# Kernel tuning notes

Hardware: AMD Instinct MI355X
Metric: run time of the kernel (lower is better)

Reference implementation:

```python
import jax, jax.numpy as jnp
import numpy as np

N_TOPICS = 256
BATCH = 131072


def setup_inputs() -> dict:
    key = jax.random.key(0)
    k = jax.random.split(key, 6)
    n, b = N_TOPICS, BATCH
    s = 1.0 / np.sqrt(n)  # matches torch RNNCell uniform(-1/sqrt(h), 1/sqrt(h)) scale
    return {
        "z": jax.random.normal(k[0], (b, n), jnp.float32),
        "h0": jax.random.uniform(k[1], (1, n), jnp.float32),
        "W_ih": jax.random.uniform(k[2], (n, n), jnp.float32, -s, s),
        "W_hh": jax.random.uniform(k[3], (n, n), jnp.float32, -s, s),
        "b_ih": jax.random.uniform(k[4], (n,), jnp.float32, -s, s),
        "b_hh": jax.random.uniform(k[5], (n,), jnp.float32, -s, s),
    }


def _stick_breaking(x):
    # torch.distributions.StickBreakingTransform._call
    D = x.shape[-1]
    offset = jnp.arange(D, 0, -1, dtype=x.dtype)          # [D, D-1, ..., 1]
    zc = jax.nn.sigmoid(x - jnp.log(offset))
    fi = jnp.finfo(x.dtype)
    zc = jnp.clip(zc, fi.tiny, 1.0 - fi.eps)              # _clipped_sigmoid
    z_cumprod = jnp.cumprod(1.0 - zc, axis=-1)
    ones = jnp.ones(x.shape[:-1] + (1,), x.dtype)
    return jnp.concatenate([zc, ones], -1) * jnp.concatenate([ones, z_cumprod], -1)


def reference(z, h0, W_ih, W_hh, b_ih, b_hh):
    n = W_ih.shape[0]
    D = n - 1
    b = b_ih + b_hh
    # step 0: rnncell(h0) with zero hidden state -> tanh(h0 @ W_ih.T + b_ih + b_hh)
    h1 = jnp.tanh(h0 @ W_ih.T + b)                        # (1, n)
    # steps i>0: rnncell(h, h) = tanh(h @ (W_ih + W_hh).T + b_ih + b_hh)
    Wc = (W_ih + W_hh).T

    def step(h, _):
        hn = jnp.tanh(h @ Wc + b)
        return hn, hn

    _, hs = jax.lax.scan(step, h1, None, length=D - 1)    # (D-1, 1, n)
    H = jnp.concatenate([h1[None], hs], axis=0)[:, 0, :]  # (D, n)
    eta = jax.nn.sigmoid(H @ z.T).T                       # (batch, D)
    return _stick_breaking(eta)                           # (batch, n)
```

## Files before the change

### kernel.cpp

```cpp
#include <hip/hip_runtime.h>

#define NTOP 256

typedef __attribute__((ext_vector_type(8))) short bf16x8;
typedef __attribute__((ext_vector_type(4))) float f32x4;

__device__ inline unsigned int packbf(float x) {
  unsigned int u = __float_as_uint(x);
  unsigned int r = (u + 0x7fffu + ((u >> 16) & 1u)) & 0xffff0000u;
  float res = x - __uint_as_float(r);
  unsigned int u2 = __float_as_uint(res);
  unsigned int r2 = u2 + 0x7fffu + ((u2 >> 16) & 1u);
  return r | (r2 >> 16);
}

__device__ inline float tanh_fast(float x) {
  float e = __expf(2.f * x);
  return 1.f - 2.f / (e + 1.f);
}

template <int CTRL>
__device__ inline float dpp_f(float v) {
  return __int_as_float(__builtin_amdgcn_update_dpp(
      0, __float_as_int(v), CTRL, 0xf, 0xf, true));
}

__global__ __launch_bounds__(1024)
__attribute__((amdgpu_waves_per_eu(4, 4)))
void rsbc_recur(
    const float* __restrict__ Wih, const float* __restrict__ Whh,
    const float* __restrict__ bih, const float* __restrict__ bhh,
    const float* __restrict__ h0, unsigned int* __restrict__ Hpack) {
  __shared__ float hA[4][68], hB[4][68];
  const int tid = threadIdx.x;
  const int j = tid >> 2, qt = tid & 3, k0 = qt * 64;
  const float bj = bih[j] + bhh[j];

  float4 w[16];
  {
    const float4* wp = reinterpret_cast<const float4*>(Wih + j * NTOP + k0);
#pragma unroll
    for (int q = 0; q < 16; ++q) w[q] = wp[q];
  }
  if (tid < NTOP) hA[tid >> 6][tid & 63] = h0[tid];
  __syncthreads();

  {
    const float* hq = hA[qt];
    float a0 = 0.f, a1 = 0.f, a2 = 0.f, a3 = 0.f;
#pragma unroll
    for (int q = 0; q < 16; ++q) {
      float4 hv = *reinterpret_cast<const float4*>(hq + 4 * q);
      a0 = fmaf(hv.x, w[q].x, a0);
      a1 = fmaf(hv.y, w[q].y, a1);
      a2 = fmaf(hv.z, w[q].z, a2);
      a3 = fmaf(hv.w, w[q].w, a3);
    }
    float sv = (a0 + a1) + (a2 + a3);
    sv += dpp_f<0xB1>(sv);
    sv += dpp_f<0x4E>(sv);
    if (qt == 0) {
      float v = tanh_fast(sv + bj);
      hB[j >> 6][j & 63] = v;
      Hpack[j] = packbf(v);
    }
  }
  {
    const float4* wq = reinterpret_cast<const float4*>(Whh + j * NTOP + k0);
#pragma unroll
    for (int q = 0; q < 16; ++q) {
      float4 t = wq[q];
      w[q].x += t.x; w[q].y += t.y; w[q].z += t.z; w[q].w += t.w;
    }
  }
  __syncthreads();

#pragma unroll 1
  for (int s = 1; s < 255; ++s) {
    const float(*hr)[68] = (s & 1) ? hB : hA;
    float(*hw)[68] = (s & 1) ? hA : hB;
    const float* hq = hr[qt];
    float a0 = 0.f, a1 = 0.f, a2 = 0.f, a3 = 0.f;
#pragma unroll
    for (int q = 0; q < 16; ++q) {
      float4 hv = *reinterpret_cast<const float4*>(hq + 4 * q);
      a0 = fmaf(hv.x, w[q].x, a0);
      a1 = fmaf(hv.y, w[q].y, a1);
      a2 = fmaf(hv.z, w[q].z, a2);
      a3 = fmaf(hv.w, w[q].w, a3);
    }
    float sv = (a0 + a1) + (a2 + a3);
    sv += dpp_f<0xB1>(sv);
    sv += dpp_f<0x4E>(sv);
    if (qt == 0) {
      float v = tanh_fast(sv + bj);
      hw[j >> 6][j & 63] = v;
      Hpack[s * NTOP + j] = packbf(v);
    }
    __syncthreads();
  }
}

__global__ __launch_bounds__(512)
__attribute__((amdgpu_waves_per_eu(2, 2)))
void rsbc_gemm_sb(
    const float* __restrict__ z, const unsigned int* __restrict__ Hpack,
    float* __restrict__ out) {
  constexpr int AS = 72;
  constexpr int BS = 72;
  constexpr int ES = 260;
  __shared__ __align__(16) char smem[135168];
  __shared__ float logtab[256];
  ushort* Ahi = reinterpret_cast<ushort*>(smem);
  ushort* Alo = Ahi + 128 * AS;
  ushort* Bhi = Alo + 128 * AS;
  ushort* Blo = Bhi + 256 * BS;
  float* eta = reinterpret_cast<float*>(smem);
  float* segT = eta + 128 * ES;

  const int tid = threadIdx.x;
  const size_t row0 = (size_t)blockIdx.x * 128;
  const int wid = tid >> 6, lane = tid & 63;
  const int wr = wid >> 2, wc = wid & 3;
  const int l15 = lane & 15, l4 = lane >> 4;

  if (tid < 255) logtab[tid] = logf((float)(255 - tid));

  f32x4 acc[4][4];
#pragma unroll
  for (int mt = 0; mt < 4; ++mt)
#pragma unroll
    for (int nt = 0; nt < 4; ++nt) acc[mt][nt] = (f32x4){0.f, 0.f, 0.f, 0.f};

  for (int kc = 0; kc < 4; ++kc) {
    const int kb = kc * 64;
    float4 zreg[4];
#pragma unroll
    for (int it = 0; it < 4; ++it) {
      int idx = tid + 512 * it;
      int r = idx >> 4, q = idx & 15;
      zreg[it] = *reinterpret_cast<const float4*>(
          z + (row0 + r) * NTOP + kb + 4 * q);
    }
    uint4 hreg[8];
#pragma unroll
    for (int it = 0; it < 8; ++it) {
      int idx = tid + 512 * it;
      int r = idx >> 4, q = idx & 15;
      hreg[it] = (r < 255)
                     ? *reinterpret_cast<const uint4*>(
                           Hpack + r * NTOP + kb + 4 * q)
                     : make_uint4(0u, 0u, 0u, 0u);
    }
    __syncthreads();
#pragma unroll
    for (int it = 0; it < 4; ++it) {
      int idx = tid + 512 * it;
      int r = idx >> 4, q = idx & 15;
      float4 v = zreg[it];
      unsigned int p0 = packbf(v.x), p1 = packbf(v.y),
                   p2 = packbf(v.z), p3 = packbf(v.w);
      *reinterpret_cast<ushort4*>(&Ahi[r * AS + 4 * q]) = make_ushort4(
          (ushort)(p0 >> 16), (ushort)(p1 >> 16),
          (ushort)(p2 >> 16), (ushort)(p3 >> 16));
      *reinterpret_cast<ushort4*>(&Alo[r * AS + 4 * q]) = make_ushort4(
          (ushort)(p0 & 0xffff), (ushort)(p1 & 0xffff),
          (ushort)(p2 & 0xffff), (ushort)(p3 & 0xffff));
    }
#pragma unroll
    for (int it = 0; it < 8; ++it) {
      int idx = tid + 512 * it;
      int r = idx >> 4, q = idx & 15;
      uint4 hv = hreg[it];
      *reinterpret_cast<ushort4*>(&Bhi[r * BS + 4 * q]) = make_ushort4(
          (ushort)(hv.x >> 16), (ushort)(hv.y >> 16),
          (ushort)(hv.z >> 16), (ushort)(hv.w >> 16));
      *reinterpret_cast<ushort4*>(&Blo[r * BS + 4 * q]) = make_ushort4(
          (ushort)(hv.x & 0xffff), (ushort)(hv.y & 0xffff),
          (ushort)(hv.z & 0xffff), (ushort)(hv.w & 0xffff));
    }
    __syncthreads();
#pragma unroll
    for (int ks = 0; ks < 2; ++ks) {
      const int ko = ks * 32 + l4 * 8;
      bf16x8 afh[4], afl[4], bfh[4], bfl[4];
#pragma unroll
      for (int mt = 0; mt < 4; ++mt) {
        int r = 64 * wr + 16 * mt + l15;
        afh[mt] = *reinterpret_cast<const bf16x8*>(&Ahi[r * AS + ko]);
        afl[mt] = *reinterpret_cast<const bf16x8*>(&Alo[r * AS + ko]);
      }
#pragma unroll
      for (int nt = 0; nt < 4; ++nt) {
        int n = 64 * wc + 16 * nt + l15;
        bfh[nt] = *reinterpret_cast<const bf16x8*>(&Bhi[n * BS + ko]);
        bfl[nt] = *reinterpret_cast<const bf16x8*>(&Blo[n * BS + ko]);
      }
#pragma unroll
      for (int mt = 0; mt < 4; ++mt)
#pragma unroll
        for (int nt = 0; nt < 4; ++nt) {
          acc[mt][nt] = __builtin_amdgcn_mfma_f32_16x16x32_bf16(
              afh[mt], bfh[nt], acc[mt][nt], 0, 0, 0);
          acc[mt][nt] = __builtin_amdgcn_mfma_f32_16x16x32_bf16(
              afh[mt], bfl[nt], acc[mt][nt], 0, 0, 0);
          acc[mt][nt] = __builtin_amdgcn_mfma_f32_16x16x32_bf16(
              afl[mt], bfh[nt], acc[mt][nt], 0, 0, 0);
        }
    }
  }
  __syncthreads();

#pragma unroll
  for (int mt = 0; mt < 4; ++mt) {
    int rbase = 64 * wr + 16 * mt + 4 * l4;
#pragma unroll
    for (int nt = 0; nt < 4; ++nt) {
      int c = 64 * wc + 16 * nt + l15;
#pragma unroll
      for (int i = 0; i < 4; ++i) {
        float x = acc[mt][nt][i];
        eta[(rbase + i) * ES + c] = 1.f / (1.f + __expf(-x));
      }
    }
  }
  __syncthreads();

  const int r = tid >> 2, qk = tid & 3;
  const int kbeg = 64 * qk, kend = (qk == 3) ? 255 : 64 * qk + 64;
  float* er = &eta[r * ES];
  {
    float cp = 1.f;
#pragma unroll 4
    for (int k = kbeg; k < kend; ++k) {
      float x = er[k] - logtab[k];
      float zc = 1.f / (1.f + __expf(-x));
      zc = fminf(fmaxf(zc, 1.1754943508222875e-38f), 0.99999988079071045f);
      er[k] = zc * cp;
      cp *= 1.f - zc;
    }
    segT[r * 4 + qk] = cp;
  }
  __syncthreads();
  {
    float p = 1.f;
    if (qk > 0) p *= segT[r * 4 + 0];
    if (qk > 1) p *= segT[r * 4 + 1];
    if (qk > 2) p *= segT[r * 4 + 2];
    if (qk > 0) {
#pragma unroll 4
      for (int k = kbeg; k < kend; ++k) er[k] *= p;
    }
    if (qk == 3) er[255] = p * segT[r * 4 + 3];
  }
  __syncthreads();

#pragma unroll
  for (int it = 0; it < 16; ++it) {
    int idx = tid + 512 * it;
    int rr = idx >> 6, cq = idx & 63;
    float4 vv = *reinterpret_cast<const float4*>(&eta[rr * ES + 4 * cq]);
    *reinterpret_cast<float4*>(&out[(row0 + rr) * NTOP + 4 * cq]) = vv;
  }
}

extern "C" void kernel_launch(void* const* d_in, const int* in_sizes, int n_in,
                              void* d_out, int out_size, void* d_ws, size_t ws_size,
                              hipStream_t stream) {
  const float* z   = (const float*)d_in[0];
  const float* h0  = (const float*)d_in[1];
  const float* Wih = (const float*)d_in[2];
  const float* Whh = (const float*)d_in[3];
  const float* bih = (const float*)d_in[4];
  const float* bhh = (const float*)d_in[5];
  float* out = (float*)d_out;
  unsigned int* Hpack = (unsigned int*)d_ws;

  rsbc_recur<<<1, 1024, 0, stream>>>(Wih, Whh, bih, bhh, h0, Hpack);
  const int nrows = out_size / NTOP;
  const int blocks = nrows / 128;
  rsbc_gemm_sb<<<blocks, 512, 0, stream>>>(z, Hpack, out);
}
```

Baseline: 323.2 us.

## Restructure recurrence thread mapping and shrink GEMM tiles for higher occupancy

The recurrence kernel now has each 16-lane group compute four output neurons over 16-element K slices. It reduces with a 16-lane DPP tree and uses a padded, swizzled shared-memory layout for h. This is meant to cut per-step LDS reads and the serial latency of the 254-step recurrence. The GEMM+stick-breaking kernel moves to 64-row tiles with a 32-wide K step, halving shared memory per block to allow 4 waves per EU. This trades more blocks and more K iterations, each with its own barriers, for higher occupancy and better latency hiding. The stick-breaking scan is split into 8 segments per row instead of 4.

```diff
diff --git a/kernel.cpp b/kernel.cpp
--- a/kernel.cpp
+++ b/kernel.cpp
@@ -25,195 +25,202 @@
       0, __float_as_int(v), CTRL, 0xf, 0xf, true));
 }
 
+__device__ inline float red16(float v) {
+  v += dpp_f<0xB1>(v);
+  v += dpp_f<0x4E>(v);
+  v += dpp_f<0x114>(v);
+  v += dpp_f<0x118>(v);
+  return v;
+}
+
 __global__ __launch_bounds__(1024)
 __attribute__((amdgpu_waves_per_eu(4, 4)))
 void rsbc_recur(
     const float* __restrict__ Wih, const float* __restrict__ Whh,
     const float* __restrict__ bih, const float* __restrict__ bhh,
     const float* __restrict__ h0, unsigned int* __restrict__ Hpack) {
-  __shared__ float hA[4][68], hB[4][68];
+  __shared__ float hA[320], hB[320];
   const int tid = threadIdx.x;
-  const int j = tid >> 2, qt = tid & 3, k0 = qt * 64;
-  const float bj = bih[j] + bhh[j];
-
-  float4 w[16];
+  const int jg = tid >> 4;
+  const int ks = tid & 15;
+  const int kb = ks * 20;
+  const int j0 = jg * 4;
+  const float b0 = bih[j0] + bhh[j0], b1 = bih[j0 + 1] + bhh[j0 + 1];
+  const float b2 = bih[j0 + 2] + bhh[j0 + 2], b3 = bih[j0 + 3] + bhh[j0 + 3];
+  const int swz = 4 * (j0 >> 4);
+
+  float4 w[4][4];
+#pragma unroll
+  for (int jj = 0; jj < 4; ++jj)
+#pragma unroll
+    for (int kq = 0; kq < 4; ++kq)
+      w[jj][kq] = *reinterpret_cast<const float4*>(
+          Wih + (j0 + jj) * NTOP + 16 * ks + 4 * kq);
+
+  if (tid < NTOP) hA[tid + 4 * (tid >> 4)] = h0[tid];
+  __syncthreads();
+
   {
-    const float4* wp = reinterpret_cast<const float4*>(Wih + j * NTOP + k0);
-#pragma unroll
-    for (int q = 0; q < 16; ++q) w[q] = wp[q];
-  }
-  if (tid < NTOP) hA[tid >> 6][tid & 63] = h0[tid];
-  __syncthreads();
-
-  {
-    const float* hq = hA[qt];
+    const float* hq = hA + kb;
+    float4 hv0 = *reinterpret_cast<const float4*>(hq);
+    float4 hv1 = *reinterpret_cast<const float4*>(hq + 4);
+    float4 hv2 = *reinterpret_cast<const float4*>(hq + 8);
+    float4 hv3 = *reinterpret_cast<const float4*>(hq + 12);
     float a0 = 0.f, a1 = 0.f, a2 = 0.f, a3 = 0.f;
-#pragma unroll
-    for (int q = 0; q < 16; ++q) {
-      float4 hv = *reinterpret_cast<const float4*>(hq + 4 * q);
-      a0 = fmaf(hv.x, w[q].x, a0);
-      a1 = fmaf(hv.y, w[q].y, a1);
-      a2 = fmaf(hv.z, w[q].z, a2);
-      a3 = fmaf(hv.w, w[q].w, a3);
-    }
-    float sv = (a0 + a1) + (a2 + a3);
-    sv += dpp_f<0xB1>(sv);
-    sv += dpp_f<0x4E>(sv);
-    if (qt == 0) {
-      float v = tanh_fast(sv + bj);
-      hB[j >> 6][j & 63] = v;
-      Hpack[j] = packbf(v);
-    }
-  }
-  {
-    const float4* wq = reinterpret_cast<const float4*>(Whh + j * NTOP + k0);
-#pragma unroll
-    for (int q = 0; q < 16; ++q) {
-      float4 t = wq[q];
-      w[q].x += t.x; w[q].y += t.y; w[q].z += t.z; w[q].w += t.w;
-    }
-  }
+#define ACC4(aj, jj)                                                        \
+  aj = fmaf(hv0.x, w[jj][0].x, aj); aj = fmaf(hv0.y, w[jj][0].y, aj);       \
+  aj = fmaf(hv0.z, w[jj][0].z, aj); aj = fmaf(hv0.w, w[jj][0].w, aj);       \
+  aj = fmaf(hv1.x, w[jj][1].x, aj); aj = fmaf(hv1.y, w[jj][1].y, aj);       \
+  aj = fmaf(hv1.z, w[jj][1].z, aj); aj = fmaf(hv1.w, w[jj][1].w, aj);       \
+  aj = fmaf(hv2.x, w[jj][2].x, aj); aj = fmaf(hv2.y, w[jj][2].y, aj);       \
+  aj = fmaf(hv2.z, w[jj][2].z, aj); aj = fmaf(hv2.w, w[jj][2].w, aj);       \
+  aj = fmaf(hv3.x, w[jj][3].x, aj); aj = fmaf(hv3.y, w[jj][3].y, aj);       \
+  aj = fmaf(hv3.z, w[jj][3].z, aj); aj = fmaf(hv3.w, w[jj][3].w, aj);
+    ACC4(a0, 0) ACC4(a1, 1) ACC4(a2, 2) ACC4(a3, 3)
+    a0 = red16(a0); a1 = red16(a1); a2 = red16(a2); a3 = red16(a3);
+    if (ks == 15) {
+      float v0 = tanh_fast(a0 + b0), v1 = tanh_fast(a1 + b1);
+      float v2 = tanh_fast(a2 + b2), v3 = tanh_fast(a3 + b3);
+      hB[j0 + swz + 0] = v0; hB[j0 + swz + 1] = v1;
+      hB[j0 + swz + 2] = v2; hB[j0 + swz + 3] = v3;
+      Hpack[j0 + 0] = packbf(v0); Hpack[j0 + 1] = packbf(v1);
+      Hpack[j0 + 2] = packbf(v2); Hpack[j0 + 3] = packbf(v3);
+    }
+  }
+#pragma unroll
+  for (int jj = 0; jj < 4; ++jj)
+#pragma unroll
+    for (int kq = 0; kq < 4; ++kq) {
+      float4 t = *reinterpret_cast<const float4*>(
+          Whh + (j0 + jj) * NTOP + 16 * ks + 4 * kq);
+      w[jj][kq].x += t.x; w[jj][kq].y += t.y;
+      w[jj][kq].z += t.z; w[jj][kq].w += t.w;
+    }
   __syncthreads();
 
 #pragma unroll 1
   for (int s = 1; s < 255; ++s) {
-    const float(*hr)[68] = (s & 1) ? hB : hA;
-    float(*hw)[68] = (s & 1) ? hA : hB;
-    const float* hq = hr[qt];
+    const float* hq = ((s & 1) ? hB : hA) + kb;
+    float* hw = (s & 1) ? hA : hB;
+    float4 hv0 = *reinterpret_cast<const float4*>(hq);
+    float4 hv1 = *reinterpret_cast<const float4*>(hq + 4);
+    float4 hv2 = *reinterpret_cast<const float4*>(hq + 8);
+    float4 hv3 = *reinterpret_cast<const float4*>(hq + 12);
     float a0 = 0.f, a1 = 0.f, a2 = 0.f, a3 = 0.f;
-#pragma unroll
-    for (int q = 0; q < 16; ++q) {
-      float4 hv = *reinterpret_cast<const float4*>(hq + 4 * q);
-      a0 = fmaf(hv.x, w[q].x, a0);
-      a1 = fmaf(hv.y, w[q].y, a1);
-      a2 = fmaf(hv.z, w[q].z, a2);
-      a3 = fmaf(hv.w, w[q].w, a3);
-    }
-    float sv = (a0 + a1) + (a2 + a3);
-    sv += dpp_f<0xB1>(sv);
-    sv += dpp_f<0x4E>(sv);
-    if (qt == 0) {
-      float v = tanh_fast(sv + bj);
-      hw[j >> 6][j & 63] = v;
-      Hpack[s * NTOP + j] = packbf(v);
+    ACC4(a0, 0) ACC4(a1, 1) ACC4(a2, 2) ACC4(a3, 3)
+    a0 = red16(a0); a1 = red16(a1); a2 = red16(a2); a3 = red16(a3);
+    if (ks == 15) {
+      float v0 = tanh_fast(a0 + b0), v1 = tanh_fast(a1 + b1);
+      float v2 = tanh_fast(a2 + b2), v3 = tanh_fast(a3 + b3);
+      hw[j0 + swz + 0] = v0; hw[j0 + swz + 1] = v1;
+      hw[j0 + swz + 2] = v2; hw[j0 + swz + 3] = v3;
+      unsigned int* hp = Hpack + s * NTOP + j0;
+      hp[0] = packbf(v0); hp[1] = packbf(v1);
+      hp[2] = packbf(v2); hp[3] = packbf(v3);
     }
     __syncthreads();
   }
+#undef ACC4
 }
 
 __global__ __launch_bounds__(512)
-__attribute__((amdgpu_waves_per_eu(2, 2)))
+__attribute__((amdgpu_waves_per_eu(4, 4)))
 void rsbc_gemm_sb(
     const float* __restrict__ z, const unsigned int* __restrict__ Hpack,
     float* __restrict__ out) {
-  constexpr int AS = 72;
-  constexpr int BS = 72;
+  constexpr int AS = 40;
   constexpr int ES = 260;
-  __shared__ __align__(16) char smem[135168];
+  __shared__ __align__(16) char smem[66560];
   __shared__ float logtab[256];
+  __shared__ float segT[64 * 8];
   ushort* Ahi = reinterpret_cast<ushort*>(smem);
-  ushort* Alo = Ahi + 128 * AS;
-  ushort* Bhi = Alo + 128 * AS;
-  ushort* Blo = Bhi + 256 * BS;
+  ushort* Alo = Ahi + 64 * AS;
+  ushort* Bhi = Alo + 64 * AS;
+  ushort* Blo = Bhi + 256 * AS;
   float* eta = reinterpret_cast<float*>(smem);
-  float* segT = eta + 128 * ES;
 
   const int tid = threadIdx.x;
-  const size_t row0 = (size_t)blockIdx.x * 128;
+  const size_t row0 = (size_t)blockIdx.x * 64;
   const int wid = tid >> 6, lane = tid & 63;
   const int wr = wid >> 2, wc = wid & 3;
   const int l15 = lane & 15, l4 = lane >> 4;
 
   if (tid < 255) logtab[tid] = logf((float)(255 - tid));
 
-  f32x4 acc[4][4];
-#pragma unroll
-  for (int mt = 0; mt < 4; ++mt)
+  f32x4 acc[2][4];
+#pragma unroll
+  for (int mt = 0; mt < 2; ++mt)
 #pragma unroll
     for (int nt = 0; nt < 4; ++nt) acc[mt][nt] = (f32x4){0.f, 0.f, 0.f, 0.f};
 
-  for (int kc = 0; kc < 4; ++kc) {
-    const int kb = kc * 64;
-    float4 zreg[4];
+  const int pr = tid >> 3, pq = tid & 7;
+
+  for (int kc = 0; kc < 8; ++kc) {
+    const int kb = kc * 32;
+    float4 zreg = *reinterpret_cast<const float4*>(
+        z + (row0 + pr) * NTOP + kb + 4 * pq);
+    uint4 hreg[4];
 #pragma unroll
     for (int it = 0; it < 4; ++it) {
       int idx = tid + 512 * it;
-      int r = idx >> 4, q = idx & 15;
-      zreg[it] = *reinterpret_cast<const float4*>(
-          z + (row0 + r) * NTOP + kb + 4 * q);
-    }
-    uint4 hreg[8];
-#pragma unroll
-    for (int it = 0; it < 8; ++it) {
-      int idx = tid + 512 * it;
-      int r = idx >> 4, q = idx & 15;
-      hreg[it] = (r < 255)
-                     ? *reinterpret_cast<const uint4*>(
-                           Hpack + r * NTOP + kb + 4 * q)
-                     : make_uint4(0u, 0u, 0u, 0u);
+      int r = idx >> 3, q = idx & 7;
+      hreg[it] = (r < 255) ? *reinterpret_cast<const uint4*>(
+                                 Hpack + r * NTOP + kb + 4 * q)
+                           : make_uint4(0u, 0u, 0u, 0u);
     }
     __syncthreads();
+    {
+      unsigned int p0 = packbf(zreg.x), p1 = packbf(zreg.y),
+                   p2 = packbf(zreg.z), p3 = packbf(zreg.w);
+      *reinterpret_cast<ushort4*>(&Ahi[pr * AS + 4 * pq]) = make_ushort4(
+          (ushort)(p0 >> 16), (ushort)(p1 >> 16),
+          (ushort)(p2 >> 16), (ushort)(p3 >> 16));
+      *reinterpret_cast<ushort4*>(&Alo[pr * AS + 4 * pq]) = make_ushort4(
+          (ushort)(p0 & 0xffff), (ushort)(p1 & 0xffff),
+          (ushort)(p2 & 0xffff), (ushort)(p3 & 0xffff));
+    }
 #pragma unroll
     for (int it = 0; it < 4; ++it) {
       int idx = tid + 512 * it;
-      int r = idx >> 4, q = idx & 15;
-      float4 v = zreg[it];
-      unsigned int p0 = packbf(v.x), p1 = packbf(v.y),
-                   p2 = packbf(v.z), p3 = packbf(v.w);
-      *reinterpret_cast<ushort4*>(&Ahi[r * AS + 4 * q]) = make_ushort4(
-          (ushort)(p0 >> 16), (ushort)(p1 >> 16),
-          (ushort)(p2 >> 16), (ushort)(p3 >> 16));
-      *reinterpret_cast<ushort4*>(&Alo[r * AS + 4 * q]) = make_ushort4(
-          (ushort)(p0 & 0xffff), (ushort)(p1 & 0xffff),
-          (ushort)(p2 & 0xffff), (ushort)(p3 & 0xffff));
-    }
-#pragma unroll
-    for (int it = 0; it < 8; ++it) {
-      int idx = tid + 512 * it;
-      int r = idx >> 4, q = idx & 15;
+      int r = idx >> 3, q = idx & 7;
       uint4 hv = hreg[it];
-      *reinterpret_cast<ushort4*>(&Bhi[r * BS + 4 * q]) = make_ushort4(
+      *reinterpret_cast<ushort4*>(&Bhi[r * AS + 4 * q]) = make_ushort4(
           (ushort)(hv.x >> 16), (ushort)(hv.y >> 16),
           (ushort)(hv.z >> 16), (ushort)(hv.w >> 16));
-      *reinterpret_cast<ushort4*>(&Blo[r * BS + 4 * q]) = make_ushort4(
+      *reinterpret_cast<ushort4*>(&Blo[r * AS + 4 * q]) = make_ushort4(
           (ushort)(hv.x & 0xffff), (ushort)(hv.y & 0xffff),
           (ushort)(hv.z & 0xffff), (ushort)(hv.w & 0xffff));
     }
     __syncthreads();
-#pragma unroll
-    for (int ks = 0; ks < 2; ++ks) {
-      const int ko = ks * 32 + l4 * 8;
-      bf16x8 afh[4], afl[4], bfh[4], bfl[4];
-#pragma unroll
-      for (int mt = 0; mt < 4; ++mt) {
-        int r = 64 * wr + 16 * mt + l15;
-        afh[mt] = *reinterpret_cast<const bf16x8*>(&Ahi[r * AS + ko]);
-        afl[mt] = *reinterpret_cast<const bf16x8*>(&Alo[r * AS + ko]);
+    const int ko = l4 * 8;
+    bf16x8 ah[2], al[2];
+#pragma unroll
+    for (int mt = 0; mt < 2; ++mt) {
+      int r = 32 * wr + 16 * mt + l15;
+      ah[mt] = *reinterpret_cast<const bf16x8*>(&Ahi[r * AS + ko]);
+      al[mt] = *reinterpret_cast<const bf16x8*>(&Alo[r * AS + ko]);
+    }
+#pragma unroll
+    for (int nt = 0; nt < 4; ++nt) {
+      int n = 64 * wc + 16 * nt + l15;
+      bf16x8 bh = *reinterpret_cast<const bf16x8*>(&Bhi[n * AS + ko]);
+      bf16x8 bl = *reinterpret_cast<const bf16x8*>(&Blo[n * AS + ko]);
+#pragma unroll
+      for (int mt = 0; mt < 2; ++mt) {
+        acc[mt][nt] = __builtin_amdgcn_mfma_f32_16x16x32_bf16(
+            ah[mt], bh, acc[mt][nt], 0, 0, 0);
+        acc[mt][nt] = __builtin_amdgcn_mfma_f32_16x16x32_bf16(
+            ah[mt], bl, acc[mt][nt], 0, 0, 0);
+        acc[mt][nt] = __builtin_amdgcn_mfma_f32_16x16x32_bf16(
+            al[mt], bh, acc[mt][nt], 0, 0, 0);
       }
-#pragma unroll
-      for (int nt = 0; nt < 4; ++nt) {
-        int n = 64 * wc + 16 * nt + l15;
-        bfh[nt] = *reinterpret_cast<const bf16x8*>(&Bhi[n * BS + ko]);
-        bfl[nt] = *reinterpret_cast<const bf16x8*>(&Blo[n * BS + ko]);
-      }
-#pragma unroll
-      for (int mt = 0; mt < 4; ++mt)
-#pragma unroll
-        for (int nt = 0; nt < 4; ++nt) {
-          acc[mt][nt] = __builtin_amdgcn_mfma_f32_16x16x32_bf16(
-              afh[mt], bfh[nt], acc[mt][nt], 0, 0, 0);
-          acc[mt][nt] = __builtin_amdgcn_mfma_f32_16x16x32_bf16(
-              afh[mt], bfl[nt], acc[mt][nt], 0, 0, 0);
-          acc[mt][nt] = __builtin_amdgcn_mfma_f32_16x16x32_bf16(
-              afl[mt], bfh[nt], acc[mt][nt], 0, 0, 0);
-        }
-    }
-  }
-  __syncthreads();
-
-#pragma unroll
-  for (int mt = 0; mt < 4; ++mt) {
-    int rbase = 64 * wr + 16 * mt + 4 * l4;
+    }
+  }
+  __syncthreads();
+
+#pragma unroll
+  for (int mt = 0; mt < 2; ++mt) {
+    int rbase = 32 * wr + 16 * mt + 4 * l4;
 #pragma unroll
     for (int nt = 0; nt < 4; ++nt) {
       int c = 64 * wc + 16 * nt + l15;
@@ -226,8 +233,8 @@
   }
   __syncthreads();
 
-  const int r = tid >> 2, qk = tid & 3;
-  const int kbeg = 64 * qk, kend = (qk == 3) ? 255 : 64 * qk + 64;
+  const int r = tid >> 3, qk = tid & 7;
+  const int kbeg = 32 * qk, kend = (qk == 7) ? 255 : 32 * qk + 32;
   float* er = &eta[r * ES];
   {
     float cp = 1.f;
@@ -239,24 +246,24 @@
       er[k] = zc * cp;
       cp *= 1.f - zc;
     }
-    segT[r * 4 + qk] = cp;
+    segT[r * 8 + qk] = cp;
   }
   __syncthreads();
   {
     float p = 1.f;
-    if (qk > 0) p *= segT[r * 4 + 0];
-    if (qk > 1) p *= segT[r * 4 + 1];
-    if (qk > 2) p *= segT[r * 4 + 2];
+#pragma unroll
+    for (int i = 0; i < 7; ++i)
+      if (i < qk) p *= segT[r * 8 + i];
     if (qk > 0) {
 #pragma unroll 4
       for (int k = kbeg; k < kend; ++k) er[k] *= p;
     }
-    if (qk == 3) er[255] = p * segT[r * 4 + 3];
-  }
-  __syncthreads();
-
-#pragma unroll
-  for (int it = 0; it < 16; ++it) {
+    if (qk == 7) er[255] = p * segT[r * 8 + 7];
+  }
+  __syncthreads();
+
+#pragma unroll
+  for (int it = 0; it < 8; ++it) {
     int idx = tid + 512 * it;
     int rr = idx >> 6, cq = idx & 63;
     float4 vv = *reinterpret_cast<const float4*>(&eta[rr * ES + 4 * cq]);
@@ -278,6 +285,6 @@
 
   rsbc_recur<<<1, 1024, 0, stream>>>(Wih, Whh, bih, bhh, h0, Hpack);
   const int nrows = out_size / NTOP;
-  const int blocks = nrows / 128;
+  const int blocks = nrows / 64;
   rsbc_gemm_sb<<<blocks, 512, 0, stream>>>(z, Hpack, out);
 }
```

New measurement: 448.0 us. 1.39x slower.
